# Optimization experiments

Hardware: AMD Instinct MI355X
Metric: run time of the kernel (lower is better)

Reference implementation:

```python
import jax, jax.numpy as jnp
import numpy as np

B, T, D, H = 256, 128, 256, 512
L = 2  # label_size


def _lstm_scan(xs, Wih, Whh, b):
    """xs: [T,B,Din]; Wih: [4H,Din]; Whh: [4H,H]; b: [4H]. Returns h_seq [T,B,H], (hT,cT).
    PyTorch LSTMCell gate order: i, f, g, o."""
    Hh = Whh.shape[1]

    def step(carry, xt):
        h, c = carry
        gates = xt @ Wih.T + h @ Whh.T + b  # [B,4H]
        i, f, g, o = jnp.split(gates, 4, axis=-1)
        c = jax.nn.sigmoid(f) * c + jax.nn.sigmoid(i) * jnp.tanh(g)
        h = jax.nn.sigmoid(o) * jnp.tanh(c)
        return (h, c), h

    Bt = xs.shape[1]
    h0 = jnp.zeros((Bt, Hh), xs.dtype)
    c0 = jnp.zeros((Bt, Hh), xs.dtype)
    (hT, cT), hs = jax.lax.scan(step, (h0, c0), xs)
    return hs, (hT, cT)


def setup_inputs() -> dict:
    key = jax.random.key(0)
    ks = jax.random.split(key, 8)

    def xavier(k, shape):
        fan_in, fan_out = shape[1], shape[0]
        std = np.sqrt(2.0 / (fan_in + fan_out))
        return jax.random.normal(k, shape, jnp.float32) * std

    return {
        "x": jax.random.normal(ks[0], (B, T, D), jnp.float32),
        "Wf_ih": xavier(ks[1], (4 * H, D)),
        "Wf_hh": xavier(ks[2], (4 * H, H)),
        "bf": jnp.zeros((4 * H,), jnp.float32),
        "Wb_ih": xavier(ks[3], (4 * H, D)),
        "Wb_hh": xavier(ks[4], (4 * H, H)),
        "bb": jnp.zeros((4 * H,), jnp.float32),
        "Ws_ih": xavier(ks[5], (8 * H, 2 * H)),
        "Ws_hh": xavier(ks[6], (8 * H, 2 * H)),
        "bs": jnp.zeros((8 * H,), jnp.float32),
        "Wl": xavier(ks[7], (L, 2 * H)),
        "bl": jnp.zeros((L,), jnp.float32),
    }


def reference(x, Wf_ih, Wf_hh, bf, Wb_ih, Wb_hh, bb, Ws_ih, Ws_hh, bs, Wl, bl):
    # Dropout is identity in eval mode (deterministic reference).
    xs = jnp.swapaxes(x, 0, 1)  # [T,B,D]
    f_seq, _ = _lstm_scan(xs, Wf_ih, Wf_hh, bf)          # forward over t=0..T-1
    b_seq, _ = _lstm_scan(xs[::-1], Wb_ih, Wb_hh, bb)    # backward over t=T-1..0, in append order
    # Faithful to source: zip(f, b) pairs f[i] with b[i] (b in reverse-time append order).
    combined = jnp.concatenate([f_seq, b_seq], axis=-1)  # [T,B,2H]
    _, (hs, _) = _lstm_scan(combined, Ws_ih, Ws_hh, bs)  # final hidden [B,2H]
    return jax.nn.sigmoid(hs @ Wl.T + bl)                # [B,L]
```

## Files before the change

kernel.cpp:

```cpp
#include <hip/hip_runtime.h>
#include <math.h>

#define BB 256
#define TT 128
#define DD 256
#define HH 512

typedef __bf16 bf16x8 __attribute__((ext_vector_type(8)));
typedef float  f32x4  __attribute__((ext_vector_type(4)));

__device__ inline unsigned short f2bf(float f) {
  unsigned u = __builtin_bit_cast(unsigned, f);
  unsigned r = (u + 0x7fffu + ((u >> 16) & 1u)) >> 16;
  return (unsigned short)r;
}
__device__ inline float bf2f(unsigned short h) {
  unsigned u = ((unsigned)h) << 16;
  return __builtin_bit_cast(float, u);
}
__device__ inline float sigm(float x)   { return 1.f / (1.f + __expf(-x)); }
__device__ inline float tanh_f(float x) { return 2.f / (1.f + __expf(-2.f * x)) - 1.f; }

__device__ __forceinline__ void gl16(const void* g, void* l) {
  __builtin_amdgcn_global_load_lds(
      (const __attribute__((address_space(1))) unsigned int*)g,
      (__attribute__((address_space(3))) unsigned int*)l, 16, 0, 0);
}

__device__ __forceinline__ void vmw8() { asm volatile("s_waitcnt vmcnt(8)" ::: "memory"); }
__device__ __forceinline__ void vmw4() { asm volatile("s_waitcnt vmcnt(4)" ::: "memory"); }
__device__ __forceinline__ void vmw0() { asm volatile("s_waitcnt vmcnt(0)" ::: "memory"); }

__global__ void prep(const float* __restrict__ x,
                     const float* __restrict__ Wf_ih, const float* __restrict__ Wf_hh, const float* __restrict__ bf_,
                     const float* __restrict__ Wb_ih, const float* __restrict__ Wb_hh, const float* __restrict__ bb_,
                     const float* __restrict__ Ws_ih, const float* __restrict__ Ws_hh, const float* __restrict__ bs_,
                     unsigned short* __restrict__ xb, unsigned short* __restrict__ Wpf,
                     unsigned short* __restrict__ Wpb, unsigned short* __restrict__ Wps,
                     float* __restrict__ bpf, float* __restrict__ bpb, float* __restrict__ bps,
                     unsigned short* __restrict__ comb, unsigned short* __restrict__ hs,
                     float* __restrict__ cf, float* __restrict__ cb, float* __restrict__ cs) {
  const long gid = (long)blockIdx.x * blockDim.x + threadIdx.x;
  const long stride = (long)gridDim.x * blockDim.x;

  for (long i = gid; i < (long)BB * TT * DD; i += stride) {
    long k = i % DD;
    long bt = i / DD;
    long t = bt % TT;
    long b = bt / TT;
    xb[(t * BB + b) * DD + k] = f2bf(x[i]);
  }
  for (long i = gid; i < 2048L * 768; i += stride) {
    int n = (int)(i / 768), k = (int)(i - (long)n * 768);
    int j = n >> 2, g = n & 3;
    float vf = (k < DD) ? Wf_ih[(size_t)(g * HH + j) * DD + k]
                        : Wf_hh[(size_t)(g * HH + j) * HH + (k - DD)];
    float vb = (k < DD) ? Wb_ih[(size_t)(g * HH + j) * DD + k]
                        : Wb_hh[(size_t)(g * HH + j) * HH + (k - DD)];
    Wpf[i] = f2bf(vf);
    Wpb[i] = f2bf(vb);
  }
  for (long i = gid; i < 4096L * 2048; i += stride) {
    int n = (int)(i >> 11), k = (int)(i & 2047);
    int j = n >> 2, g = n & 3;
    float v = (k < 1024) ? Ws_ih[(size_t)(g * 1024 + j) * 1024 + k]
                         : Ws_hh[(size_t)(g * 1024 + j) * 1024 + (k - 1024)];
    Wps[i] = f2bf(v);
  }
  for (long i = gid; i < 2048; i += stride) {
    int j = (int)(i >> 2), g = (int)(i & 3);
    bpf[i] = bf_[g * HH + j];
    bpb[i] = bb_[g * HH + j];
  }
  for (long i = gid; i < 4096; i += stride) {
    int j = (int)(i >> 2), g = (int)(i & 3);
    bps[i] = bs_[g * 1024 + j];
  }
  for (long i = gid; i < (long)BB * 1024; i += stride) comb[i] = 0;
  for (long i = gid; i < 2L * BB * 1024; i += stride) hs[i] = 0;
  for (long i = gid; i < (long)BB * HH; i += stride) { cf[i] = 0.f; cb[i] = 0.f; }
  for (long i = gid; i < (long)BB * 1024; i += stride) cs[i] = 0.f;
}

template<int NKS, int KSPLIT>
__device__ __forceinline__ void gemm_tile_lds(
    const unsigned short* __restrict__ a0, long as0,
    const unsigned short* __restrict__ a1, long as1,
    const unsigned short* __restrict__ wb, long ws,
    char* sm, int tid, f32x4 (&acc)[4]) {
  const int rl   = tid >> 3;
  const int eb   = (tid & 7) * 16;
  const int kel  = (eb ^ ((rl & 7) << 4)) >> 1;
  const int wuni = (tid >> 6) * 1024;

  const int lane = tid & 63;
  const int w    = tid >> 6;
  const int ln   = lane & 15;
  const int q    = lane >> 4;
  const int swzr = (ln & 7) << 4;
  const int col  = w * 16 + ln;

  auto stage = [&](int buf, int k0) {
    char* lA = sm + buf * 16384;
    char* lB = lA + 8192;
    const unsigned short* ab = (k0 < KSPLIT) ? (a0 + k0) : (a1 + (k0 - KSPLIT));
    const long astr = (k0 < KSPLIT) ? as0 : as1;
#pragma unroll
    for (int h = 0; h < 2; ++h) {
      const int row = h * 32 + rl;
      gl16(ab + (long)row * astr + kel, lA + h * 4096 + wuni);
      gl16(wb + (long)row * ws + k0 + kel, lB + h * 4096 + wuni);
    }
  };

  stage(0, 0); stage(1, 64); stage(2, 128);

#pragma unroll 3
  for (int ks = 0; ks < NKS; ++ks) {
    if (ks < NKS - 2)       vmw8();
    else if (ks == NKS - 2) vmw4();
    else                    vmw0();
    __builtin_amdgcn_sched_barrier(0);
    __builtin_amdgcn_s_barrier();
    __builtin_amdgcn_sched_barrier(0);
    const char* lA = sm + (ks % 3) * 16384;
    const char* lB = lA + 8192;
#pragma unroll
    for (int ks2 = 0; ks2 < 2; ++ks2) {
      const int eo = (ks2 * 64 + q * 16) ^ swzr;
      const bf16x8 bf = *reinterpret_cast<const bf16x8*>(lB + col * 128 + eo);
#pragma unroll
      for (int mb = 0; mb < 4; ++mb) {
        const bf16x8 af = *reinterpret_cast<const bf16x8*>(lA + (mb * 16 + ln) * 128 + eo);
        acc[mb] = __builtin_amdgcn_mfma_f32_16x16x32_bf16(af, bf, acc[mb], 0, 0, 0);
      }
    }
    __builtin_amdgcn_sched_barrier(0);
    __builtin_amdgcn_s_barrier();
    __builtin_amdgcn_sched_barrier(0);
    if (ks + 3 < NKS) stage(ks % 3, (ks + 3) * 64);
  }
}

__global__ __launch_bounds__(256, 3) void phase(int p,
    const unsigned short* __restrict__ xb,
    const unsigned short* __restrict__ Wpf, const unsigned short* __restrict__ Wpb,
    const float* __restrict__ bpf, const float* __restrict__ bpb,
    unsigned short* __restrict__ comb, float* __restrict__ cf, float* __restrict__ cb,
    const unsigned short* __restrict__ Wps, const float* __restrict__ bps,
    float* __restrict__ Gs, unsigned short* __restrict__ hs, float* __restrict__ cs) {
  __shared__ __align__(16) char sm[49152];
  const int bi = blockIdx.x;
  const int tid = threadIdx.x;
  const int w = tid >> 6;
  const int lane = tid & 63;
  const int q = lane >> 4;
  const int ln = lane & 15;
  const int col = w * 16 + ln;
  float* scratch = (float*)sm;

  if (bi < 256) {
    const int t = p;
    if (t >= TT) return;
    const int xcd = bi & 7;
    const int idx = bi >> 3;
    const int m0 = (idx & 3) * 64;
    const int slot = idx >> 2;
    const int panel = xcd * 8 + slot;
    const int dir = panel & 1;
    const int n0 = (panel >> 1) * 64;
    const unsigned short* __restrict__ W = dir ? Wpb : Wpf;
    const float* __restrict__ bias = dir ? bpb : bpf;
    float* __restrict__ cbuf = dir ? cb : cf;
    const int dofs = dir ? HH : 0;
    const int tx = dir ? (TT - 1 - t) : t;

    f32x4 acc[4];
#pragma unroll
    for (int mb = 0; mb < 4; ++mb) acc[mb] = (f32x4){0.f, 0.f, 0.f, 0.f};
    gemm_tile_lds<768 / 64, DD>(
        xb + ((long)tx * BB + m0) * DD, DD,
        comb + ((long)t * BB + m0) * 1024 + dofs, 1024,
        W + (long)n0 * 768, 768, sm, tid, acc);

#pragma unroll
    for (int mb = 0; mb < 4; ++mb)
#pragma unroll
      for (int r = 0; r < 4; ++r)
        scratch[(mb * 16 + q * 4 + r) * 68 + col] = acc[mb][r];
    __syncthreads();

#pragma unroll
    for (int r = 0; r < 4; ++r) {
      const int cid = tid + r * 256;
      const int bl = cid >> 4;
      const int jl = cid & 15;
      const int b = m0 + bl;
      const int j = (n0 >> 2) + jl;
      const f32x4 g  = *reinterpret_cast<const f32x4*>(&scratch[bl * 68 + jl * 4]);
      const f32x4 bv = *reinterpret_cast<const f32x4*>(&bias[n0 + jl * 4]);
      const float gi = g[0] + bv[0];
      const float gf = g[1] + bv[1];
      const float gg = g[2] + bv[2];
      const float go = g[3] + bv[3];
      const float c_old = cbuf[(size_t)b * HH + j];
      const float c_new = sigm(gf) * c_old + sigm(gi) * tanh_f(gg);
      const float h = sigm(go) * tanh_f(c_new);
      cbuf[(size_t)b * HH + j] = c_new;
      comb[((size_t)(t + 1) * BB + b) * 1024 + dofs + j] = f2bf(h);
    }
  } else if (bi < 512) {
    if (p < 1 || p > TT) return;
    const int bb2 = bi - 256;
    const int xcd = bb2 & 7;
    const int idx = bb2 >> 3;
    const int m0 = (idx & 3) * 64;
    const int n0 = (xcd * 8 + (idx >> 2)) * 64;

    f32x4 acc[4];
#pragma unroll
    for (int mb = 0; mb < 4; ++mb) acc[mb] = (f32x4){0.f, 0.f, 0.f, 0.f};
    const unsigned short* ca = comb + ((long)p * BB + m0) * 1024;
    gemm_tile_lds<1024 / 64, 2048>(ca, 1024, ca, 1024,
                                   Wps + (long)n0 * 2048, 2048, sm, tid, acc);

    float* __restrict__ G = Gs + (size_t)((p - 1) & 1) * BB * 4096;
#pragma unroll
    for (int mb = 0; mb < 4; ++mb)
#pragma unroll
      for (int r = 0; r < 4; ++r) {
        const int row = m0 + mb * 16 + q * 4 + r;
        G[(size_t)row * 4096 + n0 + col] = acc[mb][r];
      }
  } else {
    if (p < 2 || p > TT + 1) return;
    const int s = p - 2;
    const int bb2 = bi - 512;
    const int xcd = bb2 & 7;
    const int idx = bb2 >> 3;
    const int m0 = (idx & 3) * 64;
    const int n0 = (xcd * 8 + (idx >> 2)) * 64;

    f32x4 acc[4];
#pragma unroll
    for (int mb = 0; mb < 4; ++mb) acc[mb] = (f32x4){0.f, 0.f, 0.f, 0.f};
    const unsigned short* ha = hs + ((long)(s & 1) * BB + m0) * 1024;
    gemm_tile_lds<1024 / 64, 2048>(ha, 1024, ha, 1024,
                                   Wps + (long)n0 * 2048 + 1024, 2048, sm, tid, acc);

#pragma unroll
    for (int mb = 0; mb < 4; ++mb)
#pragma unroll
      for (int r = 0; r < 4; ++r)
        scratch[(mb * 16 + q * 4 + r) * 68 + col] = acc[mb][r];
    __syncthreads();

    const float* __restrict__ G = Gs + (size_t)(s & 1) * BB * 4096;
#pragma unroll
    for (int r = 0; r < 4; ++r) {
      const int cid = tid + r * 256;
      const int bl = cid >> 4;
      const int jl = cid & 15;
      const int b = m0 + bl;
      const int j = (n0 >> 2) + jl;
      const f32x4 g   = *reinterpret_cast<const f32x4*>(&scratch[bl * 68 + jl * 4]);
      const f32x4 gin = *reinterpret_cast<const f32x4*>(&G[(size_t)b * 4096 + n0 + jl * 4]);
      const f32x4 bv  = *reinterpret_cast<const f32x4*>(&bps[n0 + jl * 4]);
      const float gi = g[0] + gin[0] + bv[0];
      const float gf = g[1] + gin[1] + bv[1];
      const float gg = g[2] + gin[2] + bv[2];
      const float go = g[3] + gin[3] + bv[3];
      const float c_old = cs[(size_t)b * 1024 + j];
      const float c_new = sigm(gf) * c_old + sigm(gi) * tanh_f(gg);
      const float h = sigm(go) * tanh_f(c_new);
      cs[(size_t)b * 1024 + j] = c_new;
      hs[((size_t)((s + 1) & 1) * BB + b) * 1024 + j] = f2bf(h);
    }
  }
}

__global__ __launch_bounds__(256) void classifier(const unsigned short* __restrict__ hs,
                                                  const float* __restrict__ Wl,
                                                  const float* __restrict__ bl,
                                                  float* __restrict__ out) {
  const int b = blockIdx.x;
  const int tid = threadIdx.x;
  const unsigned short* hb = hs + (size_t)b * 1024;
  float s0 = 0.f, s1 = 0.f;
#pragma unroll
  for (int kk = 0; kk < 4; ++kk) {
    const int k = tid * 4 + kk;
    const float hv = bf2f(hb[k]);
    s0 += hv * Wl[k];
    s1 += hv * Wl[1024 + k];
  }
  for (int off = 32; off > 0; off >>= 1) {
    s0 += __shfl_down(s0, off);
    s1 += __shfl_down(s1, off);
  }
  __shared__ float red[8];
  const int w = tid >> 6;
  if ((tid & 63) == 0) { red[w * 2] = s0; red[w * 2 + 1] = s1; }
  __syncthreads();
  if (tid == 0) {
    const float l0 = red[0] + red[2] + red[4] + red[6] + bl[0];
    const float l1 = red[1] + red[3] + red[5] + red[7] + bl[1];
    out[b * 2 + 0] = sigm(l0);
    out[b * 2 + 1] = sigm(l1);
  }
}

extern "C" void kernel_launch(void* const* d_in, const int* in_sizes, int n_in,
                              void* d_out, int out_size, void* d_ws, size_t ws_size,
                              hipStream_t stream) {
  const float* x     = (const float*)d_in[0];
  const float* Wf_ih = (const float*)d_in[1];
  const float* Wf_hh = (const float*)d_in[2];
  const float* bf_   = (const float*)d_in[3];
  const float* Wb_ih = (const float*)d_in[4];
  const float* Wb_hh = (const float*)d_in[5];
  const float* bb_   = (const float*)d_in[6];
  const float* Ws_ih = (const float*)d_in[7];
  const float* Ws_hh = (const float*)d_in[8];
  const float* bs_   = (const float*)d_in[9];
  const float* Wl    = (const float*)d_in[10];
  const float* bl    = (const float*)d_in[11];
  float* out = (float*)d_out;

  char* ws = (char*)d_ws;
  size_t off = 0;
  auto take = [&](size_t bytes) -> void* {
    void* p = ws + off;
    off += (bytes + 255) & ~(size_t)255;
    return p;
  };
  unsigned short* xb   = (unsigned short*)take((size_t)BB * TT * DD * 2);
  unsigned short* Wpf  = (unsigned short*)take((size_t)2048 * 768 * 2);
  unsigned short* Wpb  = (unsigned short*)take((size_t)2048 * 768 * 2);
  unsigned short* Wps  = (unsigned short*)take((size_t)4096 * 2048 * 2);
  float* bpf = (float*)take(2048 * 4);
  float* bpb = (float*)take(2048 * 4);
  float* bps = (float*)take(4096 * 4);
  unsigned short* comb = (unsigned short*)take((size_t)(TT + 1) * BB * 1024 * 2);
  unsigned short* hs   = (unsigned short*)take((size_t)2 * BB * 1024 * 2);
  float* cf = (float*)take((size_t)BB * HH * 4);
  float* cb = (float*)take((size_t)BB * HH * 4);
  float* cs = (float*)take((size_t)BB * 1024 * 4);
  float* Gs = (float*)take((size_t)2 * BB * 4096 * 4);

  prep<<<2048, 256, 0, stream>>>(x, Wf_ih, Wf_hh, bf_, Wb_ih, Wb_hh, bb_,
                                 Ws_ih, Ws_hh, bs_, xb, Wpf, Wpb, Wps,
                                 bpf, bpb, bps, comb, hs, cf, cb, cs);
  for (int p = 0; p < TT + 2; ++p)
    phase<<<768, 256, 0, stream>>>(p, xb, Wpf, Wpb, bpf, bpb, comb, cf, cb,
                                   Wps, bps, Gs, hs, cs);
  classifier<<<256, 256, 0, stream>>>(hs, Wl, bl, out);
}
```

Measured before the change: 1.763 ms.

## Enlarge phase GEMM tiles to 128x128 with 512-thread blocks

Every phase GEMM tile grows from 64x64 to 128x128. Each block now has 8 waves laid out 2x4, and each wave computes a 64x32 sub-tile, so two MFMAs reuse every A fragment loaded from LDS. The LDS ring buffer doubles, the per-step launch drops from 768 blocks to 192, and the epilogue is remapped to the wider scratch tile. The goal is more operand reuse and less redundant weight and activation traffic, at the cost of fewer blocks than CUs and lower occupancy on a latency-bound recurrent step.

```diff
diff --git a/kernel.cpp b/kernel.cpp
--- a/kernel.cpp
+++ b/kernel.cpp
@@ -87,29 +87,30 @@
     const unsigned short* __restrict__ a0, long as0,
     const unsigned short* __restrict__ a1, long as1,
     const unsigned short* __restrict__ wb, long ws,
-    char* sm, int tid, f32x4 (&acc)[4]) {
+    char* sm, int tid, f32x4 (&acc)[4][2]) {
   const int rl   = tid >> 3;
   const int eb   = (tid & 7) * 16;
   const int kel  = (eb ^ ((rl & 7) << 4)) >> 1;
-  const int wuni = (tid >> 6) * 1024;
+  const int wuni = ((tid >> 6) & 7) * 1024;
 
   const int lane = tid & 63;
   const int w    = tid >> 6;
+  const int wm   = w >> 2;
+  const int wn   = w & 3;
   const int ln   = lane & 15;
   const int q    = lane >> 4;
   const int swzr = (ln & 7) << 4;
-  const int col  = w * 16 + ln;
 
   auto stage = [&](int buf, int k0) {
-    char* lA = sm + buf * 16384;
-    char* lB = lA + 8192;
+    char* lA = sm + buf * 32768;
+    char* lB = lA + 16384;
     const unsigned short* ab = (k0 < KSPLIT) ? (a0 + k0) : (a1 + (k0 - KSPLIT));
     const long astr = (k0 < KSPLIT) ? as0 : as1;
 #pragma unroll
     for (int h = 0; h < 2; ++h) {
-      const int row = h * 32 + rl;
-      gl16(ab + (long)row * astr + kel, lA + h * 4096 + wuni);
-      gl16(wb + (long)row * ws + k0 + kel, lB + h * 4096 + wuni);
+      const int row = h * 64 + rl;
+      gl16(ab + (long)row * astr + kel, lA + h * 8192 + wuni);
+      gl16(wb + (long)row * ws + k0 + kel, lB + h * 8192 + wuni);
     }
   };
 
@@ -123,16 +124,24 @@
     __builtin_amdgcn_sched_barrier(0);
     __builtin_amdgcn_s_barrier();
     __builtin_amdgcn_sched_barrier(0);
-    const char* lA = sm + (ks % 3) * 16384;
-    const char* lB = lA + 8192;
+    const char* lA = sm + (ks % 3) * 32768;
+    const char* lB = lA + 16384;
 #pragma unroll
     for (int ks2 = 0; ks2 < 2; ++ks2) {
       const int eo = (ks2 * 64 + q * 16) ^ swzr;
-      const bf16x8 bf = *reinterpret_cast<const bf16x8*>(lB + col * 128 + eo);
+      bf16x8 bf[2];
+#pragma unroll
+      for (int nf = 0; nf < 2; ++nf) {
+        const int bcol = wn * 32 + nf * 16 + ln;
+        bf[nf] = *reinterpret_cast<const bf16x8*>(lB + bcol * 128 + eo);
+      }
 #pragma unroll
       for (int mb = 0; mb < 4; ++mb) {
-        const bf16x8 af = *reinterpret_cast<const bf16x8*>(lA + (mb * 16 + ln) * 128 + eo);
-        acc[mb] = __builtin_amdgcn_mfma_f32_16x16x32_bf16(af, bf, acc[mb], 0, 0, 0);
+        const int arow = wm * 64 + mb * 16 + ln;
+        const bf16x8 af = *reinterpret_cast<const bf16x8*>(lA + arow * 128 + eo);
+#pragma unroll
+        for (int nf = 0; nf < 2; ++nf)
+          acc[mb][nf] = __builtin_amdgcn_mfma_f32_16x16x32_bf16(af, bf[nf], acc[mb][nf], 0, 0, 0);
       }
     }
     __builtin_amdgcn_sched_barrier(0);
@@ -142,42 +151,46 @@
   }
 }
 
-__global__ __launch_bounds__(256, 3) void phase(int p,
+__global__ __launch_bounds__(512, 1) void phase(int p,
     const unsigned short* __restrict__ xb,
     const unsigned short* __restrict__ Wpf, const unsigned short* __restrict__ Wpb,
     const float* __restrict__ bpf, const float* __restrict__ bpb,
     unsigned short* __restrict__ comb, float* __restrict__ cf, float* __restrict__ cb,
     const unsigned short* __restrict__ Wps, const float* __restrict__ bps,
     float* __restrict__ Gs, unsigned short* __restrict__ hs, float* __restrict__ cs) {
-  __shared__ __align__(16) char sm[49152];
+  __shared__ __align__(16) char sm[98304];
   const int bi = blockIdx.x;
   const int tid = threadIdx.x;
   const int w = tid >> 6;
   const int lane = tid & 63;
   const int q = lane >> 4;
   const int ln = lane & 15;
-  const int col = w * 16 + ln;
+  const int wm = w >> 2;
+  const int wn = w & 3;
   float* scratch = (float*)sm;
 
-  if (bi < 256) {
+  if (bi < 64) {
     const int t = p;
     if (t >= TT) return;
-    const int xcd = bi & 7;
-    const int idx = bi >> 3;
-    const int m0 = (idx & 3) * 64;
-    const int slot = idx >> 2;
-    const int panel = xcd * 8 + slot;
+    const int gi = bi;
+    const int xcd = gi & 7;
+    const int rest = gi >> 3;
+    const int m0 = (rest & 1) * 128;
+    const int slot = rest >> 1;
+    const int panel = xcd * 4 + slot;
     const int dir = panel & 1;
-    const int n0 = (panel >> 1) * 64;
+    const int n0 = (panel >> 1) * 128;
     const unsigned short* __restrict__ W = dir ? Wpb : Wpf;
     const float* __restrict__ bias = dir ? bpb : bpf;
     float* __restrict__ cbuf = dir ? cb : cf;
     const int dofs = dir ? HH : 0;
     const int tx = dir ? (TT - 1 - t) : t;
 
-    f32x4 acc[4];
-#pragma unroll
-    for (int mb = 0; mb < 4; ++mb) acc[mb] = (f32x4){0.f, 0.f, 0.f, 0.f};
+    f32x4 acc[4][2];
+#pragma unroll
+    for (int mb = 0; mb < 4; ++mb)
+#pragma unroll
+      for (int nf = 0; nf < 2; ++nf) acc[mb][nf] = (f32x4){0.f, 0.f, 0.f, 0.f};
     gemm_tile_lds<768 / 64, DD>(
         xb + ((long)tx * BB + m0) * DD, DD,
         comb + ((long)t * BB + m0) * 1024 + dofs, 1024,
@@ -186,40 +199,44 @@
 #pragma unroll
     for (int mb = 0; mb < 4; ++mb)
 #pragma unroll
-      for (int r = 0; r < 4; ++r)
-        scratch[(mb * 16 + q * 4 + r) * 68 + col] = acc[mb][r];
+      for (int nf = 0; nf < 2; ++nf)
+#pragma unroll
+        for (int r = 0; r < 4; ++r)
+          scratch[(wm * 64 + mb * 16 + q * 4 + r) * 132 + wn * 32 + nf * 16 + ln] = acc[mb][nf][r];
     __syncthreads();
 
 #pragma unroll
-    for (int r = 0; r < 4; ++r) {
-      const int cid = tid + r * 256;
-      const int bl = cid >> 4;
-      const int jl = cid & 15;
+    for (int r = 0; r < 8; ++r) {
+      const int cid = tid + r * 512;
+      const int bl = cid >> 5;
+      const int jl = cid & 31;
       const int b = m0 + bl;
       const int j = (n0 >> 2) + jl;
-      const f32x4 g  = *reinterpret_cast<const f32x4*>(&scratch[bl * 68 + jl * 4]);
+      const f32x4 g  = *reinterpret_cast<const f32x4*>(&scratch[bl * 132 + jl * 4]);
       const f32x4 bv = *reinterpret_cast<const f32x4*>(&bias[n0 + jl * 4]);
-      const float gi = g[0] + bv[0];
+      const float gi2 = g[0] + bv[0];
       const float gf = g[1] + bv[1];
       const float gg = g[2] + bv[2];
       const float go = g[3] + bv[3];
       const float c_old = cbuf[(size_t)b * HH + j];
-      const float c_new = sigm(gf) * c_old + sigm(gi) * tanh_f(gg);
+      const float c_new = sigm(gf) * c_old + sigm(gi2) * tanh_f(gg);
       const float h = sigm(go) * tanh_f(c_new);
       cbuf[(size_t)b * HH + j] = c_new;
       comb[((size_t)(t + 1) * BB + b) * 1024 + dofs + j] = f2bf(h);
     }
-  } else if (bi < 512) {
+  } else if (bi < 128) {
     if (p < 1 || p > TT) return;
-    const int bb2 = bi - 256;
-    const int xcd = bb2 & 7;
-    const int idx = bb2 >> 3;
-    const int m0 = (idx & 3) * 64;
-    const int n0 = (xcd * 8 + (idx >> 2)) * 64;
-
-    f32x4 acc[4];
-#pragma unroll
-    for (int mb = 0; mb < 4; ++mb) acc[mb] = (f32x4){0.f, 0.f, 0.f, 0.f};
+    const int gi = bi - 64;
+    const int xcd = gi & 7;
+    const int rest = gi >> 3;
+    const int m0 = (rest & 1) * 128;
+    const int n0 = (xcd * 4 + (rest >> 1)) * 128;
+
+    f32x4 acc[4][2];
+#pragma unroll
+    for (int mb = 0; mb < 4; ++mb)
+#pragma unroll
+      for (int nf = 0; nf < 2; ++nf) acc[mb][nf] = (f32x4){0.f, 0.f, 0.f, 0.f};
     const unsigned short* ca = comb + ((long)p * BB + m0) * 1024;
     gemm_tile_lds<1024 / 64, 2048>(ca, 1024, ca, 1024,
                                    Wps + (long)n0 * 2048, 2048, sm, tid, acc);
@@ -228,22 +245,26 @@
 #pragma unroll
     for (int mb = 0; mb < 4; ++mb)
 #pragma unroll
-      for (int r = 0; r < 4; ++r) {
-        const int row = m0 + mb * 16 + q * 4 + r;
-        G[(size_t)row * 4096 + n0 + col] = acc[mb][r];
-      }
+      for (int nf = 0; nf < 2; ++nf)
+#pragma unroll
+        for (int r = 0; r < 4; ++r) {
+          const int row = m0 + wm * 64 + mb * 16 + q * 4 + r;
+          G[(size_t)row * 4096 + n0 + wn * 32 + nf * 16 + ln] = acc[mb][nf][r];
+        }
   } else {
     if (p < 2 || p > TT + 1) return;
     const int s = p - 2;
-    const int bb2 = bi - 512;
-    const int xcd = bb2 & 7;
-    const int idx = bb2 >> 3;
-    const int m0 = (idx & 3) * 64;
-    const int n0 = (xcd * 8 + (idx >> 2)) * 64;
-
-    f32x4 acc[4];
-#pragma unroll
-    for (int mb = 0; mb < 4; ++mb) acc[mb] = (f32x4){0.f, 0.f, 0.f, 0.f};
+    const int gi = bi - 128;
+    const int xcd = gi & 7;
+    const int rest = gi >> 3;
+    const int m0 = (rest & 1) * 128;
+    const int n0 = (xcd * 4 + (rest >> 1)) * 128;
+
+    f32x4 acc[4][2];
+#pragma unroll
+    for (int mb = 0; mb < 4; ++mb)
+#pragma unroll
+      for (int nf = 0; nf < 2; ++nf) acc[mb][nf] = (f32x4){0.f, 0.f, 0.f, 0.f};
     const unsigned short* ha = hs + ((long)(s & 1) * BB + m0) * 1024;
     gemm_tile_lds<1024 / 64, 2048>(ha, 1024, ha, 1024,
                                    Wps + (long)n0 * 2048 + 1024, 2048, sm, tid, acc);
@@ -251,27 +272,29 @@
 #pragma unroll
     for (int mb = 0; mb < 4; ++mb)
 #pragma unroll
-      for (int r = 0; r < 4; ++r)
-        scratch[(mb * 16 + q * 4 + r) * 68 + col] = acc[mb][r];
+      for (int nf = 0; nf < 2; ++nf)
+#pragma unroll
+        for (int r = 0; r < 4; ++r)
+          scratch[(wm * 64 + mb * 16 + q * 4 + r) * 132 + wn * 32 + nf * 16 + ln] = acc[mb][nf][r];
     __syncthreads();
 
     const float* __restrict__ G = Gs + (size_t)(s & 1) * BB * 4096;
 #pragma unroll
-    for (int r = 0; r < 4; ++r) {
-      const int cid = tid + r * 256;
-      const int bl = cid >> 4;
-      const int jl = cid & 15;
+    for (int r = 0; r < 8; ++r) {
+      const int cid = tid + r * 512;
+      const int bl = cid >> 5;
+      const int jl = cid & 31;
       const int b = m0 + bl;
       const int j = (n0 >> 2) + jl;
-      const f32x4 g   = *reinterpret_cast<const f32x4*>(&scratch[bl * 68 + jl * 4]);
+      const f32x4 g   = *reinterpret_cast<const f32x4*>(&scratch[bl * 132 + jl * 4]);
       const f32x4 gin = *reinterpret_cast<const f32x4*>(&G[(size_t)b * 4096 + n0 + jl * 4]);
       const f32x4 bv  = *reinterpret_cast<const f32x4*>(&bps[n0 + jl * 4]);
-      const float gi = g[0] + gin[0] + bv[0];
+      const float gi2 = g[0] + gin[0] + bv[0];
       const float gf = g[1] + gin[1] + bv[1];
       const float gg = g[2] + gin[2] + bv[2];
       const float go = g[3] + gin[3] + bv[3];
       const float c_old = cs[(size_t)b * 1024 + j];
-      const float c_new = sigm(gf) * c_old + sigm(gi) * tanh_f(gg);
+      const float c_new = sigm(gf) * c_old + sigm(gi2) * tanh_f(gg);
       const float h = sigm(go) * tanh_f(c_new);
       cs[(size_t)b * 1024 + j] = c_new;
       hs[((size_t)((s + 1) & 1) * BB + b) * 1024 + j] = f2bf(h);
@@ -352,7 +375,7 @@
                                  Ws_ih, Ws_hh, bs_, xb, Wpf, Wpb, Wps,
                                  bpf, bpb, bps, comb, hs, cf, cb, cs);
   for (int p = 0; p < TT + 2; ++p)
-    phase<<<768, 256, 0, stream>>>(p, xb, Wpf, Wpb, bpf, bpb, comb, cf, cb,
+    phase<<<192, 512, 0, stream>>>(p, xb, Wpf, Wpb, bpf, bpb, comb, cf, cb,
                                    Wps, bps, Gs, hs, cs);
   classifier<<<256, 256, 0, stream>>>(hs, Wl, bl, out);
 }
```

Result: slower. 1.976 ms (+12.1%).
